# Performance work log

Hardware: AMD Instinct MI355X
Metric: run time of the kernel (lower is better)

Reference implementation:

```python
import jax, jax.numpy as jnp
import numpy as np

NUM_CLASSES = 80
NUM_QUERIES = 300
TOPK = 100
B, HM, WM = 2, 200, 200


def setup_inputs() -> dict:
    key = jax.random.key(0)
    k1, k2, k3 = jax.random.split(key, 3)
    return {
        "masks_queries_logits": jax.random.normal(k1, (B, NUM_QUERIES, HM, WM), dtype=jnp.float32),
        "class_queries_logits": jax.random.normal(k2, (B, NUM_QUERIES, NUM_CLASSES), dtype=jnp.float32),
        "pred_boxes": jax.random.uniform(k3, (B, NUM_QUERIES, 4), dtype=jnp.float32),
        "h": 800,
        "w": 800,
    }


def _predict_one(mask_pred, mask_cls, boxes, h, w):
    # mask_pred: [Q, Hm, Wm], mask_cls: [Q, C], boxes: [Q, 4] cxcywh in [0,1]
    C = mask_cls.shape[-1]
    scores = jax.nn.sigmoid(mask_cls).reshape(-1)              # [Q*C]
    scores_pi, topk_idx = jax.lax.top_k(scores, TOPK)          # torch uses sorted=False; same set
    labels_pi = topk_idx % C                                   # class ids
    q_idx = topk_idx // C                                      # query ids
    mp = mask_pred[q_idx]                                      # [k, Hm, Wm]
    bx = boxes[q_idx]                                          # [k, 4]
    # bilinear upsample, align_corners=False (half-pixel centers)
    pm = jax.image.resize(mp, (TOPK, h, w), method="bilinear")  # [k, h, w] logits
    binm = (pm > 0).astype(pm.dtype)
    obj = (jax.nn.sigmoid(pm) * binm).sum((1, 2)) / (binm.sum((1, 2)) + 1e-6)
    pred_scores = scores_pi * obj
    cx, cy, bw, bh = bx[:, 0], bx[:, 1], bx[:, 2], bx[:, 3]
    fw = jnp.asarray(w, pm.dtype)
    fh = jnp.asarray(h, pm.dtype)
    x1 = jnp.clip((cx - bw / 2) * fw, 0.0, fw - 1)
    y1 = jnp.clip((cy - bh / 2) * fh, 0.0, fh - 1)
    x2 = jnp.clip((cx + bw / 2) * fw, 0.0, fw - 1)
    y2 = jnp.clip((cy + bh / 2) * fh, 0.0, fh - 1)
    boxes_xyxy = jnp.stack([x1, y1, x2, y2], axis=-1)          # [k, 4]
    pred_masks = pm > 0                                        # [k, h, w] bool
    area = (x2 - x1) * (y2 - y1)
    keep = (pred_masks.sum((1, 2)) > 5) & (area > 10) & (pred_scores > 0.05)
    boxes_scores = jnp.concatenate([boxes_xyxy, pred_scores[:, None]], axis=1)  # [k, 5]
    return boxes_scores, labels_pi, pred_masks, keep


def reference(masks_queries_logits, class_queries_logits, pred_boxes, h, w):
    fn = jax.vmap(lambda mp, mc, bx: _predict_one(mp, mc, bx, h, w))
    boxes_scores, labels, masks, keep = fn(masks_queries_logits, class_queries_logits, pred_boxes)
    # Fixed shapes for jit; `keep` is the boolean filter torch applies per image.
    return boxes_scores, labels, masks, keep
```

## Files before the change

kernel.cpp:

```cpp
#include <hip/hip_runtime.h>

typedef unsigned long long ull;
typedef float f32x4 __attribute__((ext_vector_type(4)));

#define BB 2
#define QQ 300
#define CC 80
#define KK 100
#define HM 200
#define WM 200

__device__ __forceinline__ void bin_select_desc(
    const int* hist, int* chunkSum, int krem,
    int* sh_sel, int* sh_acc)
{
    const int tid = threadIdx.x;
    if (tid < 256) {
        int cs = 0;
        #pragma unroll
        for (int j = 0; j < 8; ++j) cs += hist[tid * 8 + j];
        chunkSum[tid] = cs;
    }
    __syncthreads();
    if (tid < 64) {
        const int l = tid;
        int s0 = chunkSum[4 * l + 0];
        int s1 = chunkSum[4 * l + 1];
        int s2 = chunkSum[4 * l + 2];
        int s3 = chunkSum[4 * l + 3];
        int sum4 = s0 + s1 + s2 + s3;
        int S = sum4;
        #pragma unroll
        for (int d = 1; d < 64; d <<= 1) {
            int up = __shfl_down(S, d);
            if (l + d < 64) S += up;
        }
        int Sn = __shfl_down(S, 1);
        bool crossing = (S >= krem) && (l == 63 || Sn < krem);
        if (crossing) {
            int acc = S - sum4;
            int c = 4 * l + 3;
            int cvals[4] = {s0, s1, s2, s3};
            #pragma unroll
            for (int cc = 3; cc >= 0; --cc) {
                int cv = cvals[cc];
                if (acc + cv >= krem) { c = 4 * l + cc; goto chunk_found; }
                acc += cv;
            }
            chunk_found:
            int sel = c * 8;
            #pragma unroll
            for (int bin = 7; bin >= 0; --bin) {
                int h2 = hist[c * 8 + bin];
                if (acc + h2 >= krem) { sel = c * 8 + bin; break; }
                acc += h2;
            }
            *sh_sel = sel;
            *sh_acc = acc;
        }
    }
}

__global__ __launch_bounds__(1024) void mdh_topk_kernel(
    const float* __restrict__ cls,
    unsigned int* __restrict__ keys_ws,
    const float* __restrict__ boxes,
    const int* __restrict__ hptr,
    const int* __restrict__ wptr,
    float* __restrict__ out,
    float* __restrict__ ws_val,
    int* __restrict__ ws_qidx,
    float* __restrict__ ws_area,
    ull* __restrict__ acc_sig,
    unsigned int* __restrict__ acc_cnt,
    unsigned int* __restrict__ done)
{
    const int b = blockIdx.x;
    const int tid = threadIdx.x;
    const int N = QQ * CC;
    const float* __restrict__ lg = cls + (size_t)b * N;
    unsigned int* __restrict__ keys = keys_ws + (size_t)b * N;

    __shared__ int hist[2048];
    __shared__ int chunkSum[256];
    __shared__ int sh_sel;
    __shared__ int sh_acc;
    __shared__ int cntG, cntE;
    __shared__ float gV[128];
    __shared__ int gI[128];
    __shared__ int eI[256];
    __shared__ int fIdx[KK];
    __shared__ float fVal[KK];

    if (tid < KK) {
        acc_sig[b * KK + tid] = 0ull;
        acc_cnt[b * KK + tid] = 0u;
        done[b * KK + tid] = 0u;
    }

    unsigned int prefix = 0u;
    int krem = KK;

    for (int t = tid; t < 2048; t += 1024) hist[t] = 0;
    __syncthreads();
    for (int i = tid; i < N; i += 1024) {
        float s = 1.0f / (1.0f + expf(-lg[i]));
        unsigned int key = __float_as_uint(s);
        keys[i] = key;
        atomicAdd(&hist[key >> 21], 1);
    }
    __syncthreads();
    bin_select_desc(hist, chunkSum, krem, &sh_sel, &sh_acc);
    __syncthreads();
    prefix = (unsigned int)sh_sel << 21;
    krem = krem - sh_acc;
    __syncthreads();

    #pragma unroll
    for (int round = 1; round < 3; ++round) {
        const int shift = (round == 1) ? 10 : 0;
        const int nbits = (round == 1) ? 11 : 10;
        const unsigned int binmask = (1u << nbits) - 1u;
        const unsigned int hmask = 0xFFFFFFFFu << (shift + nbits);

        for (int t = tid; t < 2048; t += 1024) hist[t] = 0;
        __syncthreads();
        for (int i = tid * 4; i < N; i += 4096) {
            uint4 kv = *(const uint4*)(keys + i);
            unsigned int ka[4] = {kv.x, kv.y, kv.z, kv.w};
            #pragma unroll
            for (int j = 0; j < 4; ++j) {
                if ((ka[j] & hmask) == (prefix & hmask))
                    atomicAdd(&hist[(ka[j] >> shift) & binmask], 1);
            }
        }
        __syncthreads();
        bin_select_desc(hist, chunkSum, krem, &sh_sel, &sh_acc);
        __syncthreads();
        prefix = prefix | ((unsigned int)sh_sel << shift);
        krem = krem - sh_acc;
        __syncthreads();
    }

    const unsigned int T = prefix;
    if (tid == 0) { cntG = 0; cntE = 0; }
    __syncthreads();
    for (int i = tid * 4; i < N; i += 4096) {
        uint4 kv = *(const uint4*)(keys + i);
        unsigned int ka[4] = {kv.x, kv.y, kv.z, kv.w};
        #pragma unroll
        for (int j = 0; j < 4; ++j) {
            unsigned int key = ka[j];
            if (key > T) {
                int p = atomicAdd(&cntG, 1);
                if (p < 128) { gV[p] = __uint_as_float(key); gI[p] = i + j; }
            } else if (key == T) {
                int p = atomicAdd(&cntE, 1);
                if (p < 256) eI[p] = i + j;
            }
        }
    }
    __syncthreads();
    const int nG = min(cntG, 128);
    const int nE = min(cntE, 256);

    if (tid < nG) {
        float v = gV[tid]; int idx = gI[tid];
        int r = 0;
        for (int j = 0; j < nG; ++j) {
            float vj = gV[j]; int ij = gI[j];
            if (vj > v || (vj == v && ij < idx)) ++r;
        }
        if (r < KK) { fIdx[r] = idx; fVal[r] = v; }
    }
    if (tid < nE) {
        int idx = eI[tid];
        int r = 0;
        for (int j = 0; j < nE; ++j) if (eI[j] < idx) ++r;
        if (r < krem && (nG + r) < KK) { fIdx[nG + r] = idx; fVal[nG + r] = __uint_as_float(T); }
    }
    __syncthreads();

    const int h = *hptr, w = *wptr;
    const float fw = (float)w, fh = (float)h;
    if (tid < KK) {
        int idx = fIdx[tid];
        float val = fVal[tid];
        int q = idx / CC;
        int label = idx - q * CC;
        int o = b * KK + tid;
        out[BB * KK * 5 + o] = (float)label;
        const float* bx = boxes + ((size_t)(b * QQ + q)) * 4;
        float cx = bx[0], cy = bx[1], bw = bx[2], bh = bx[3];
        float x1 = fminf(fmaxf((cx - bw * 0.5f) * fw, 0.0f), fw - 1.0f);
        float y1 = fminf(fmaxf((cy - bh * 0.5f) * fh, 0.0f), fh - 1.0f);
        float x2 = fminf(fmaxf((cx + bw * 0.5f) * fw, 0.0f), fw - 1.0f);
        float y2 = fminf(fmaxf((cy + bh * 0.5f) * fh, 0.0f), fh - 1.0f);
        float* br = out + (size_t)o * 5;
        br[0] = x1; br[1] = y1; br[2] = x2; br[3] = y2;
        ws_val[o] = val;
        ws_qidx[o] = q;
        ws_area[o] = (x2 - x1) * (y2 - y1);
    }
}

__global__ __launch_bounds__(256) void mdh_masks800_kernel(
    const float* __restrict__ mp,
    const int* __restrict__ ws_qidx,
    const float* __restrict__ ws_val,
    const float* __restrict__ ws_area,
    float* __restrict__ out,
    ull* __restrict__ acc_sig,
    unsigned int* __restrict__ acc_cnt,
    unsigned int* __restrict__ done)
{
    const int orig = blockIdx.x;
    const int wg = (orig & 7) * 3925 + (orig >> 3);
    const int bq = wg / 157;
    const int chunk = wg - bq * 157;

    const int b = bq / KK;
    const int q = ws_qidx[bq];
    const float* __restrict__ src = mp + ((size_t)(b * QQ + q)) * (HM * WM);
    float* __restrict__ out_masks = out + BB * KK * 6;

    const int t = chunk * 256 + threadIdx.x;
    float ssum = 0.0f;
    int scnt = 0;

    if (t < HM * WM) {
        const int m = t / WM;
        const int k = t - m * WM;
        const int rm1 = (m > 0 ? m - 1 : 0) * WM;
        const int r0  = m * WM;
        const int rp1 = (m < HM - 1 ? m + 1 : HM - 1) * WM;
        const int cm1 = (k > 0 ? k - 1 : 0);
        const int cp1 = (k < WM - 1 ? k + 1 : WM - 1);

        float a0m = src[rm1 + cm1], a00 = src[rm1 + k], a0p = src[rm1 + cp1];
        float a1m = src[r0  + cm1], a10 = src[r0  + k], a1p = src[r0  + cp1];
        float a2m = src[rp1 + cm1], a20 = src[rp1 + k], a2p = src[rp1 + cp1];

        float* dst = out_masks + (size_t)bq * 640000 + (size_t)(4 * m) * 800 + 4 * k;

        #pragma unroll
        for (int r = 0; r < 4; ++r) {
            float um, u0, up;
            if (r == 0)      { um = 0.375f*a0m + 0.625f*a1m; u0 = 0.375f*a00 + 0.625f*a10; up = 0.375f*a0p + 0.625f*a1p; }
            else if (r == 1) { um = 0.125f*a0m + 0.875f*a1m; u0 = 0.125f*a00 + 0.875f*a10; up = 0.125f*a0p + 0.875f*a1p; }
            else if (r == 2) { um = 0.875f*a1m + 0.125f*a2m; u0 = 0.875f*a10 + 0.125f*a20; up = 0.875f*a1p + 0.125f*a2p; }
            else             { um = 0.625f*a1m + 0.375f*a2m; u0 = 0.625f*a10 + 0.375f*a20; up = 0.625f*a1p + 0.375f*a2p; }

            float pmv[4];
            pmv[0] = 0.375f * um + 0.625f * u0;
            pmv[1] = 0.125f * um + 0.875f * u0;
            pmv[2] = 0.875f * u0 + 0.125f * up;
            pmv[3] = 0.625f * u0 + 0.375f * up;

            f32x4 ov;
            #pragma unroll
            for (int j = 0; j < 4; ++j) {
                bool pos = pmv[j] > 0.0f;
                ov[j] = pos ? 1.0f : 0.0f;
                if (pos) { ssum += 1.0f / (1.0f + __expf(-pmv[j])); scnt++; }
            }
            __builtin_nontemporal_store(ov, (f32x4*)(dst + r * 800));
        }
    }

    for (int off = 32; off > 0; off >>= 1) {
        ssum += __shfl_down(ssum, off);
        scnt += __shfl_down(scnt, off);
    }
    __shared__ float wsum[4];
    __shared__ int wcnt[4];
    const int wid = threadIdx.x >> 6;
    const int lane = threadIdx.x & 63;
    if (lane == 0) { wsum[wid] = ssum; wcnt[wid] = scnt; }
    __syncthreads();
    if (threadIdx.x == 0) {
        float tt = wsum[0] + wsum[1] + wsum[2] + wsum[3];
        int c = wcnt[0] + wcnt[1] + wcnt[2] + wcnt[3];
        if (c > 0) {
            atomicAdd(&acc_sig[bq], (ull)((double)tt * 4294967296.0 + 0.5));
            atomicAdd(&acc_cnt[bq], (unsigned int)c);
        }
        asm volatile("s_waitcnt vmcnt(0)" ::: "memory");
        unsigned int old = atomicAdd(&done[bq], 1u);
        if (old == 156u) {
            ull sig_fp = atomicAdd(&acc_sig[bq], 0ull);
            unsigned int cnt = atomicAdd(&acc_cnt[bq], 0u);
            float sig = (float)((double)sig_fp * (1.0 / 4294967296.0));
            float obj = sig / ((float)cnt + 1e-6f);
            float ps = ws_val[bq] * obj;
            out[(size_t)bq * 5 + 4] = ps;
            bool keep = (cnt > 5u) && (ws_area[bq] > 10.0f) && (ps > 0.05f);
            out[(size_t)(BB * KK * 6) + (size_t)BB * KK * 640000 + bq] = keep ? 1.0f : 0.0f;
        }
    }
}

__global__ __launch_bounds__(256) void mdh_masks_kernel(
    const float* __restrict__ mp,
    const int* __restrict__ ws_qidx,
    const int* __restrict__ hptr,
    const int* __restrict__ wptr,
    float* __restrict__ out_masks,
    ull* __restrict__ acc_sig,
    unsigned int* __restrict__ acc_cnt)
{
    const int bq = blockIdx.y;
    const int b = bq / KK;
    const int q = ws_qidx[bq];
    const int h = *hptr, w = *wptr;
    const long long pix = (long long)h * w;
    const float* __restrict__ src = mp + ((size_t)(b * QQ + q)) * (HM * WM);
    const float sy = (float)HM / (float)h;
    const float sx = (float)WM / (float)w;

    const long long p0 = (long long)blockIdx.x * 1024 + (long long)threadIdx.x * 4;
    float ssum = 0.0f;
    int scnt = 0;
    if (p0 < pix) {
        float pmv[4];
        for (int j = 0; j < 4; ++j) {
            long long p = p0 + j;
            if (p >= pix) { pmv[j] = -1.0f; continue; }
            int yy = (int)(p / w);
            int xx = (int)(p - (long long)yy * w);
            float yi = ((float)yy + 0.5f) * sy - 0.5f;
            float rf = floorf(yi); float fy = yi - rf;
            int r0 = max((int)rf, 0); int r1 = min((int)rf + 1, HM - 1);
            float xi = ((float)xx + 0.5f) * sx - 0.5f;
            float cf = floorf(xi); float fx = xi - cf;
            int c0 = max((int)cf, 0); int c1 = min((int)cf + 1, WM - 1);
            float a  = src[r0 * WM + c0], b2 = src[r0 * WM + c1];
            float c  = src[r1 * WM + c0], d2 = src[r1 * WM + c1];
            float t0 = (1.0f - fy) * a  + fy * c;
            float t1 = (1.0f - fy) * b2 + fy * d2;
            pmv[j] = (1.0f - fx) * t0 + fx * t1;
        }
        for (int j = 0; j < 4; ++j) {
            long long p = p0 + j;
            if (p >= pix) continue;
            bool pos = pmv[j] > 0.0f;
            out_masks[(size_t)bq * pix + p] = pos ? 1.0f : 0.0f;
            if (pos) { ssum += 1.0f / (1.0f + __expf(-pmv[j])); scnt++; }
        }
    }

    for (int off = 32; off > 0; off >>= 1) {
        ssum += __shfl_down(ssum, off);
        scnt += __shfl_down(scnt, off);
    }
    __shared__ float wsum[4];
    __shared__ int wcnt[4];
    const int wid = threadIdx.x >> 6;
    const int lane = threadIdx.x & 63;
    if (lane == 0) { wsum[wid] = ssum; wcnt[wid] = scnt; }
    __syncthreads();
    if (threadIdx.x == 0) {
        float tt = wsum[0] + wsum[1] + wsum[2] + wsum[3];
        int c = wcnt[0] + wcnt[1] + wcnt[2] + wcnt[3];
        if (c > 0) {
            atomicAdd(&acc_sig[bq], (ull)((double)tt * 4294967296.0 + 0.5));
            atomicAdd(&acc_cnt[bq], (unsigned int)c);
        }
    }
}

__global__ void mdh_final_kernel(
    const ull* __restrict__ acc_sig,
    const unsigned int* __restrict__ acc_cnt,
    const float* __restrict__ ws_val,
    const float* __restrict__ ws_area,
    float* __restrict__ out,
    long long pix)
{
    int t = blockIdx.x * blockDim.x + threadIdx.x;
    if (t < BB * KK) {
        float sig = (float)((double)acc_sig[t] * (1.0 / 4294967296.0));
        unsigned int cnt = acc_cnt[t];
        float obj = sig / ((float)cnt + 1e-6f);
        float ps = ws_val[t] * obj;
        out[(size_t)t * 5 + 4] = ps;
        bool keep = (cnt > 5) && (ws_area[t] > 10.0f) && (ps > 0.05f);
        out[(size_t)(BB * KK * 5 + BB * KK) + (size_t)BB * KK * pix + t] = keep ? 1.0f : 0.0f;
    }
}

extern "C" void kernel_launch(void* const* d_in, const int* in_sizes, int n_in,
                              void* d_out, int out_size, void* d_ws, size_t ws_size,
                              hipStream_t stream)
{
    const float* mp    = (const float*)d_in[0];
    const float* cls   = (const float*)d_in[1];
    const float* boxes = (const float*)d_in[2];
    const int* hptr    = (const int*)d_in[3];
    const int* wptr    = (const int*)d_in[4];
    float* out = (float*)d_out;

    const long long pix = ((long long)out_size - (long long)BB * KK * 7) / ((long long)BB * KK);

    char* wsb = (char*)d_ws;
    ull* acc_sig          = (ull*)wsb;
    unsigned int* acc_cnt = (unsigned int*)(wsb + 1600);
    float* ws_val         = (float*)(wsb + 2400);
    int* ws_qidx          = (int*)(wsb + 3200);
    float* ws_area        = (float*)(wsb + 4000);
    unsigned int* ws_done = (unsigned int*)(wsb + 4800);
    unsigned int* ws_keys = (unsigned int*)(wsb + 5600);

    mdh_topk_kernel<<<BB, 1024, 0, stream>>>(cls, ws_keys, boxes, hptr, wptr, out,
                                             ws_val, ws_qidx, ws_area,
                                             acc_sig, acc_cnt, ws_done);

    if (pix == 640000) {
        mdh_masks800_kernel<<<200 * 157, 256, 0, stream>>>(
            mp, ws_qidx, ws_val, ws_area, out, acc_sig, acc_cnt, ws_done);
    } else {
        const int nblk = (int)((pix + 1023) / 1024);
        mdh_masks_kernel<<<dim3(nblk, BB * KK), 256, 0, stream>>>(
            mp, ws_qidx, hptr, wptr, out + BB * KK * 6, acc_sig, acc_cnt);
        mdh_final_kernel<<<1, 256, 0, stream>>>(acc_sig, acc_cnt, ws_val, ws_area, out, pix);
    }
}
```

Before: 129.1 us.

## Compute eight output rows per thread and replace atomic finalize with reduce kernel

Each thread of the 800x800 mask kernel now handles two source rows (eight output rows), loading a 4x3 neighbourhood instead of a 3x3 one per source row, which halves the block count and cuts redundant source loads. The per-block atomic accumulation with a last-block-done finalize is replaced by writing per-block partial sums to a workspace, followed by a single-block reduce kernel that computes objectness, score and keep. This removes global atomics and the done-counter handshake, but adds a kernel launch and changes the summation from fixed-point to float order.

```diff
diff --git a/kernel.cpp b/kernel.cpp
--- a/kernel.cpp
+++ b/kernel.cpp
@@ -9,6 +9,9 @@
 #define KK 100
 #define HM 200
 #define WM 200
+
+#define BLKS_PER_BQ 79
+#define NBLK800 (200 * BLKS_PER_BQ)
 
 __device__ __forceinline__ void bin_select_desc(
     const int* hist, int* chunkSum, int krem,
@@ -72,8 +75,7 @@
     int* __restrict__ ws_qidx,
     float* __restrict__ ws_area,
     ull* __restrict__ acc_sig,
-    unsigned int* __restrict__ acc_cnt,
-    unsigned int* __restrict__ done)
+    unsigned int* __restrict__ acc_cnt)
 {
     const int b = blockIdx.x;
     const int tid = threadIdx.x;
@@ -95,7 +97,6 @@
     if (tid < KK) {
         acc_sig[b * KK + tid] = 0ull;
         acc_cnt[b * KK + tid] = 0u;
-        done[b * KK + tid] = 0u;
     }
 
     unsigned int prefix = 0u;
@@ -207,49 +208,50 @@
 __global__ __launch_bounds__(256) void mdh_masks800_kernel(
     const float* __restrict__ mp,
     const int* __restrict__ ws_qidx,
-    const float* __restrict__ ws_val,
-    const float* __restrict__ ws_area,
-    float* __restrict__ out,
-    ull* __restrict__ acc_sig,
-    unsigned int* __restrict__ acc_cnt,
-    unsigned int* __restrict__ done)
+    float* __restrict__ out_masks,
+    float2* __restrict__ partials)
 {
     const int orig = blockIdx.x;
-    const int wg = (orig & 7) * 3925 + (orig >> 3);
-    const int bq = wg / 157;
-    const int chunk = wg - bq * 157;
+    const int wg = (orig & 7) * (NBLK800 / 8) + (orig >> 3);
+    const int bq = wg / BLKS_PER_BQ;
+    const int chunk = wg - bq * BLKS_PER_BQ;
 
     const int b = bq / KK;
     const int q = ws_qidx[bq];
     const float* __restrict__ src = mp + ((size_t)(b * QQ + q)) * (HM * WM);
-    float* __restrict__ out_masks = out + BB * KK * 6;
 
     const int t = chunk * 256 + threadIdx.x;
     float ssum = 0.0f;
     int scnt = 0;
 
-    if (t < HM * WM) {
-        const int m = t / WM;
-        const int k = t - m * WM;
-        const int rm1 = (m > 0 ? m - 1 : 0) * WM;
-        const int r0  = m * WM;
-        const int rp1 = (m < HM - 1 ? m + 1 : HM - 1) * WM;
+    if (t < 100 * WM) {
+        const int u = t / WM;
+        const int k = t - u * WM;
+        const int rA = (u > 0 ? 2 * u - 1 : 0) * WM;
+        const int rB = (2 * u) * WM;
+        const int rC = (2 * u + 1) * WM;
+        const int rD = (u < 99 ? 2 * u + 2 : HM - 1) * WM;
         const int cm1 = (k > 0 ? k - 1 : 0);
         const int cp1 = (k < WM - 1 ? k + 1 : WM - 1);
 
-        float a0m = src[rm1 + cm1], a00 = src[rm1 + k], a0p = src[rm1 + cp1];
-        float a1m = src[r0  + cm1], a10 = src[r0  + k], a1p = src[r0  + cp1];
-        float a2m = src[rp1 + cm1], a20 = src[rp1 + k], a2p = src[rp1 + cp1];
-
-        float* dst = out_masks + (size_t)bq * 640000 + (size_t)(4 * m) * 800 + 4 * k;
+        float Am = src[rA + cm1], A0 = src[rA + k], Ap = src[rA + cp1];
+        float Bm = src[rB + cm1], B0 = src[rB + k], Bp = src[rB + cp1];
+        float Cm = src[rC + cm1], C0 = src[rC + k], Cp = src[rC + cp1];
+        float Dm = src[rD + cm1], D0 = src[rD + k], Dp = src[rD + cp1];
+
+        float* dst = out_masks + (size_t)bq * 640000 + (size_t)(8 * u) * 800 + 4 * k;
 
         #pragma unroll
-        for (int r = 0; r < 4; ++r) {
+        for (int rr = 0; rr < 8; ++rr) {
             float um, u0, up;
-            if (r == 0)      { um = 0.375f*a0m + 0.625f*a1m; u0 = 0.375f*a00 + 0.625f*a10; up = 0.375f*a0p + 0.625f*a1p; }
-            else if (r == 1) { um = 0.125f*a0m + 0.875f*a1m; u0 = 0.125f*a00 + 0.875f*a10; up = 0.125f*a0p + 0.875f*a1p; }
-            else if (r == 2) { um = 0.875f*a1m + 0.125f*a2m; u0 = 0.875f*a10 + 0.125f*a20; up = 0.875f*a1p + 0.125f*a2p; }
-            else             { um = 0.625f*a1m + 0.375f*a2m; u0 = 0.625f*a10 + 0.375f*a20; up = 0.625f*a1p + 0.375f*a2p; }
+            if (rr == 0)      { um = 0.375f*Am + 0.625f*Bm; u0 = 0.375f*A0 + 0.625f*B0; up = 0.375f*Ap + 0.625f*Bp; }
+            else if (rr == 1) { um = 0.125f*Am + 0.875f*Bm; u0 = 0.125f*A0 + 0.875f*B0; up = 0.125f*Ap + 0.875f*Bp; }
+            else if (rr == 2) { um = 0.875f*Bm + 0.125f*Cm; u0 = 0.875f*B0 + 0.125f*C0; up = 0.875f*Bp + 0.125f*Cp; }
+            else if (rr == 3) { um = 0.625f*Bm + 0.375f*Cm; u0 = 0.625f*B0 + 0.375f*C0; up = 0.625f*Bp + 0.375f*Cp; }
+            else if (rr == 4) { um = 0.375f*Bm + 0.625f*Cm; u0 = 0.375f*B0 + 0.625f*C0; up = 0.375f*Bp + 0.625f*Cp; }
+            else if (rr == 5) { um = 0.125f*Bm + 0.875f*Cm; u0 = 0.125f*B0 + 0.875f*C0; up = 0.125f*Bp + 0.875f*Cp; }
+            else if (rr == 6) { um = 0.875f*Cm + 0.125f*Dm; u0 = 0.875f*C0 + 0.125f*D0; up = 0.875f*Cp + 0.125f*Dp; }
+            else              { um = 0.625f*Cm + 0.375f*Dm; u0 = 0.625f*C0 + 0.375f*D0; up = 0.625f*Cp + 0.375f*Dp; }
 
             float pmv[4];
             pmv[0] = 0.375f * um + 0.625f * u0;
@@ -264,7 +266,7 @@
                 ov[j] = pos ? 1.0f : 0.0f;
                 if (pos) { ssum += 1.0f / (1.0f + __expf(-pmv[j])); scnt++; }
             }
-            __builtin_nontemporal_store(ov, (f32x4*)(dst + r * 800));
+            __builtin_nontemporal_store(ov, (f32x4*)(dst + rr * 800));
         }
     }
 
@@ -281,22 +283,27 @@
     if (threadIdx.x == 0) {
         float tt = wsum[0] + wsum[1] + wsum[2] + wsum[3];
         int c = wcnt[0] + wcnt[1] + wcnt[2] + wcnt[3];
-        if (c > 0) {
-            atomicAdd(&acc_sig[bq], (ull)((double)tt * 4294967296.0 + 0.5));
-            atomicAdd(&acc_cnt[bq], (unsigned int)c);
-        }
-        asm volatile("s_waitcnt vmcnt(0)" ::: "memory");
-        unsigned int old = atomicAdd(&done[bq], 1u);
-        if (old == 156u) {
-            ull sig_fp = atomicAdd(&acc_sig[bq], 0ull);
-            unsigned int cnt = atomicAdd(&acc_cnt[bq], 0u);
-            float sig = (float)((double)sig_fp * (1.0 / 4294967296.0));
-            float obj = sig / ((float)cnt + 1e-6f);
-            float ps = ws_val[bq] * obj;
-            out[(size_t)bq * 5 + 4] = ps;
-            bool keep = (cnt > 5u) && (ws_area[bq] > 10.0f) && (ps > 0.05f);
-            out[(size_t)(BB * KK * 6) + (size_t)BB * KK * 640000 + bq] = keep ? 1.0f : 0.0f;
-        }
+        partials[wg] = make_float2(tt, (float)c);
+    }
+}
+
+__global__ __launch_bounds__(256) void mdh_reduce_kernel(
+    const float2* __restrict__ partials,
+    const float* __restrict__ ws_val,
+    const float* __restrict__ ws_area,
+    float* __restrict__ out)
+{
+    int bq = threadIdx.x;
+    if (bq < BB * KK) {
+        const float2* p = partials + bq * BLKS_PER_BQ;
+        float s = 0.0f, c = 0.0f;
+        #pragma unroll 4
+        for (int i = 0; i < BLKS_PER_BQ; ++i) { float2 v = p[i]; s += v.x; c += v.y; }
+        float obj = s / (c + 1e-6f);
+        float ps = ws_val[bq] * obj;
+        out[(size_t)bq * 5 + 4] = ps;
+        bool keep = (c > 5.0f) && (ws_area[bq] > 10.0f) && (ps > 0.05f);
+        out[(size_t)(BB * KK * 6) + (size_t)BB * KK * 640000 + bq] = keep ? 1.0f : 0.0f;
     }
 }
 
@@ -408,16 +415,16 @@
     float* ws_val         = (float*)(wsb + 2400);
     int* ws_qidx          = (int*)(wsb + 3200);
     float* ws_area        = (float*)(wsb + 4000);
-    unsigned int* ws_done = (unsigned int*)(wsb + 4800);
-    unsigned int* ws_keys = (unsigned int*)(wsb + 5600);
+    float2* ws_partials   = (float2*)(wsb + 4800);
+    unsigned int* ws_keys = (unsigned int*)(wsb + 131200);
 
     mdh_topk_kernel<<<BB, 1024, 0, stream>>>(cls, ws_keys, boxes, hptr, wptr, out,
-                                             ws_val, ws_qidx, ws_area,
-                                             acc_sig, acc_cnt, ws_done);
+                                             ws_val, ws_qidx, ws_area, acc_sig, acc_cnt);
 
     if (pix == 640000) {
-        mdh_masks800_kernel<<<200 * 157, 256, 0, stream>>>(
-            mp, ws_qidx, ws_val, ws_area, out, acc_sig, acc_cnt, ws_done);
+        mdh_masks800_kernel<<<NBLK800, 256, 0, stream>>>(
+            mp, ws_qidx, out + BB * KK * 6, ws_partials);
+        mdh_reduce_kernel<<<1, 256, 0, stream>>>(ws_partials, ws_val, ws_area, out);
     } else {
         const int nblk = (int)((pix + 1023) / 1024);
         mdh_masks_kernel<<<dim3(nblk, BB * KK), 256, 0, stream>>>(
```

After: 152.1 us. +17.8%, slower.
